# Performance work log

Measured on AMD Instinct MI355X. Metric: run time of the kernel, lower is better.

Reference implementation:

```python
import jax, jax.numpy as jnp
import numpy as np

DEPTH = 6

def sparsemax(z):
    # sparsemax over last axis (Martins & Astudillo 2016)
    z_sorted = -jnp.sort(-z, axis=-1)
    z_cum = jnp.cumsum(z_sorted, axis=-1)
    k = jnp.arange(1, z.shape[-1] + 1, dtype=z.dtype)
    support = k * z_sorted > z_cum - 1.0
    k_sup = jnp.sum(support, axis=-1, keepdims=True).astype(jnp.int32)
    tau_sum = jnp.take_along_axis(z_cum, k_sup - 1, axis=-1)
    tau = (tau_sum - 1.0) / k_sup.astype(z.dtype)
    return jnp.maximum(z - tau, 0.0)

def sparsemoid(x):
    return jnp.clip(0.5 * x + 0.5, 0.0, 1.0)

def make_bin_codes(depth):
    indices = jnp.arange(2 ** depth)
    offsets = 2 ** jnp.arange(depth)
    bin_codes = ((indices[None, :] // offsets[:, None]) % 2).astype(jnp.float32)
    return jnp.stack([bin_codes, 1.0 - bin_codes], axis=-1)  # [depth, 2^depth, 2]

def odste_forward(x, fsl, esl, thr, lt, resp, codes):
    # x: [B,J,D]; fsl: [n,t,J]; esl: [n,t,J,D]; thr/lt: [n,t]; resp: [n,c,D,2^t]
    fs = sparsemax(fsl)                               # [n,t,J]
    es = sparsemax(esl)                               # [n,t,J,D]
    sel = jnp.einsum('bjd,ntj->bntd', x, fs)          # feature selection
    sel = sel * jnp.sum(es, axis=2)[None]             # einsum 'bntd,ntjd->bntd'
    tl = (sel - thr[None, :, :, None]) * jnp.exp(-lt)[None, :, :, None]
    tl = jnp.stack([-tl, tl], axis=-1)                # [b,n,t,d,2]
    bins = sparsemoid(tl)
    bm = jnp.einsum('bntds,tcs->bntdc', bins, codes)  # [b,n,t,d,c]
    rw = jnp.prod(bm, axis=2)                         # [b,n,d,c]
    return jnp.einsum('bnds,ncds->bnd', rw, resp)     # [b,n,d]


def setup_inputs() -> dict:
    key = jax.random.key(0)
    B, D, n, t, c_tree = 64, 32, 128, DEPTH, 1
    Js = [64, 192, 320]
    ks = jax.random.split(key, 1 + 5 * len(Js))
    inp = {'x': jax.random.normal(ks[0], (B, Js[0], D), dtype=jnp.float32)}
    for i, J in enumerate(Js):
        k0, k1, k2, k3, k4 = ks[1 + 5 * i:6 + 5 * i]
        inp[f'fsl_{i}'] = jax.random.uniform(k0, (n, t, J), dtype=jnp.float32)
        inp[f'esl_{i}'] = jax.random.normal(k1, (n, t, J, D), dtype=jnp.float32)
        inp[f'thr_{i}'] = jax.random.normal(k2, (n, t), dtype=jnp.float32)
        inp[f'lt_{i}'] = jax.random.normal(k3, (n, t), dtype=jnp.float32)
        inp[f'resp_{i}'] = jax.random.normal(k4, (n, c_tree, D, 2 ** t), dtype=jnp.float32)
    return inp


def reference(x, fsl_0, esl_0, thr_0, lt_0, resp_0,
              fsl_1, esl_1, thr_1, lt_1, resp_1,
              fsl_2, esl_2, thr_2, lt_2, resp_2):
    codes = make_bin_codes(DEPTH)
    layers = [(fsl_0, esl_0, thr_0, lt_0, resp_0),
              (fsl_1, esl_1, thr_1, lt_1, resp_1),
              (fsl_2, esl_2, thr_2, lt_2, resp_2)]
    for fsl, esl, thr, lt, resp in layers:
        h = odste_forward(x, fsl, esl, thr, lt, resp, codes)
        x = jnp.concatenate([x, h], axis=1)
    return x
```

## Files before the change

### kernel.cpp

```cpp
#include <hip/hip_runtime.h>

#define OUT_COLS 448
#define OUT_STRIDE (OUT_COLS * 32)
#define NTREES 128
#define TDEPTH 6
#define NT (NTREES * TDEPTH)
#define DD 32
#define BB 64
#define PADW 64

template <int CTRL, int RMASK = 0xf, bool BC = true>
__device__ __forceinline__ float dppf(float v) {
    return __int_as_float(
        __builtin_amdgcn_update_dpp(0, __float_as_int(v), CTRL, RMASK, 0xf, BC));
}

__device__ __forceinline__ float wred64(float x) {
    x += dppf<0x111>(x);
    x += dppf<0x112>(x);
    x += dppf<0x114>(x);
    x += dppf<0x118>(x);
    x += __int_as_float(__builtin_amdgcn_update_dpp(0, __float_as_int(x), 0x142, 0xa, 0xf, false));
    x += __int_as_float(__builtin_amdgcn_update_dpp(0, __float_as_int(x), 0x143, 0xc, 0xf, false));
    return __int_as_float(__builtin_amdgcn_readlane(__float_as_int(x), 63));
}

template <int J>
__device__ __forceinline__ void fs_row(const float* __restrict__ zr, int lane,
                                       float2* __restrict__ fjv, int* __restrict__ fcnt_p) {
    constexpr int T = J / 64;
    float z[T];
    #pragma unroll
    for (int t = 0; t < T; ++t) z[t] = zr[t * 64 + lane];
    float sp = 0.f;
    #pragma unroll
    for (int t = 0; t < T; ++t) sp += z[t];
    float k = (float)J;
    float tau = (wred64(sp) - 1.f) / k;
    #pragma unroll 1
    for (int it = 0; it < 64; ++it) {
        float s2 = 0.f, c2 = 0.f;
        #pragma unroll
        for (int t = 0; t < T; ++t) {
            bool g = z[t] > tau;
            s2 += g ? z[t] : 0.f;
            c2 += g ? 1.f : 0.f;
        }
        float S2 = wred64(s2);
        float K2 = wred64(c2);
        if (K2 == k) break;
        k = K2;
        tau = (S2 - 1.f) / K2;
    }
    unsigned long long below = (1ull << lane) - 1ull;
    int base = 0;
    #pragma unroll
    for (int t = 0; t < T; ++t) {
        bool sup = z[t] > tau;
        unsigned long long m = __ballot(sup);
        int pos = base + __popcll(m & below);
        if (sup && pos < PADW)
            fjv[pos] = make_float2(__int_as_float((t * 64 + lane) * 128), z[t] - tau);
        base += __popcll(m);
    }
    int cnt = base < PADW ? base : PADW;
    for (int i = cnt + lane; i < PADW; i += 64)
        fjv[i] = make_float2(__int_as_float(0), 0.f);
    if (lane == 0) *fcnt_p = cnt;
}

template <int S>
__device__ __forceinline__ void bstep(float* a, int lane) {
    constexpr int half = 16 >> S;
    bool up = ((lane >> S) & 1) != 0;
    #pragma unroll
    for (int q = 0; q < half; ++q) {
        float send = up ? a[q] : a[half + q];
        float recv;
        if constexpr (S == 0)      recv = dppf<0xB1>(send);
        else if constexpr (S == 1) recv = dppf<0x4E>(send);
        else recv = __int_as_float(__builtin_amdgcn_ds_swizzle(
                        __float_as_int(send), ((1 << S) << 10) | 0x1F));
        float keep = up ? a[half + q] : a[q];
        a[q] = keep + recv;
    }
}

__global__ __launch_bounds__(256)
void prep_kernel(const float* __restrict__ x,
                 const float* __restrict__ f0, const float* __restrict__ f1,
                 const float* __restrict__ f2,
                 const float* __restrict__ e0, const float* __restrict__ e1,
                 const float* __restrict__ e2,
                 float2* __restrict__ fjv, int* __restrict__ fcnt,
                 float* __restrict__ part, float* __restrict__ out) {
    int w = blockIdx.x * 4 + (threadIdx.x >> 6);
    int lane = threadIdx.x & 63;

    if (w < 512) {
        const float4* x4 = (const float4*)x;
        float4* o4 = (float4*)out;
        int g = w * 64 + lane;
        int b = g >> 9, r = g & 511;
        o4[(size_t)b * (OUT_STRIDE / 4) + r] = x4[g];
        return;
    }
    w -= 512;
    if (w < 3 * NT) {
        if (w < NT) {
            fs_row<64>(f0 + (size_t)w * 64, lane, fjv + (size_t)w * PADW, fcnt + w);
        } else if (w < 2 * NT) {
            int r = w - NT;
            fs_row<192>(f1 + (size_t)r * 192, lane,
                        fjv + (size_t)(NT + r) * PADW, fcnt + NT + r);
        } else {
            int r = w - 2 * NT;
            fs_row<320>(f2 + (size_t)r * 320, lane,
                        fjv + (size_t)(2 * NT + r) * PADW, fcnt + 2 * NT + r);
        }
        return;
    }
    w -= 3 * NT;
    const float* esl; int row, chunk, J; size_t grow;
    if (w < NT)          { esl = e0; row = w; chunk = 0; J = 64; grow = (size_t)row; }
    else if (w < 4 * NT) { int q = w - NT; esl = e1; row = q / 3; chunk = q - row * 3; J = 192; grow = (size_t)(NT + row); }
    else                 { int q = w - 4 * NT; esl = e2; row = q / 5; chunk = q - row * 5; J = 320; grow = (size_t)(2 * NT + row); }

    const float4* zp4 = (const float4*)(esl + ((size_t)row * J + chunk * 64 + lane) * 32);
    float z[32];
    #pragma unroll
    for (int i = 0; i < 8; ++i) {
        float4 v = zp4[i];
        z[4 * i] = v.x; z[4 * i + 1] = v.y; z[4 * i + 2] = v.z; z[4 * i + 3] = v.w;
    }
    float mx = z[0];
    #pragma unroll
    for (int i = 1; i < 32; ++i) mx = fmaxf(mx, z[i]);
    float tau = mx - 1.0f;
    int kprev = -1;
    #pragma unroll 1
    for (int it = 0; it < 40; ++it) {
        float s0 = 0.f, s1 = 0.f, s2 = 0.f, s3 = 0.f;
        int k0 = 0, k1 = 0, k2 = 0, k3 = 0;
        #pragma unroll
        for (int i = 0; i < 8; ++i) {
            bool g0 = z[4 * i]     > tau; s0 += g0 ? z[4 * i]     : 0.f; k0 += g0;
            bool g1 = z[4 * i + 1] > tau; s1 += g1 ? z[4 * i + 1] : 0.f; k1 += g1;
            bool g2 = z[4 * i + 2] > tau; s2 += g2 ? z[4 * i + 2] : 0.f; k2 += g2;
            bool g3 = z[4 * i + 3] > tau; s3 += g3 ? z[4 * i + 3] : 0.f; k3 += g3;
        }
        float S = (s0 + s1) + (s2 + s3);
        int k = (k0 + k1) + (k2 + k3);
        bool chg = (k != kprev);
        kprev = k;
        tau = (S - 1.0f) / (float)k;
        if (__ballot(chg) == 0ull) break;
    }
    #pragma unroll
    for (int i = 0; i < 32; ++i) z[i] = fmaxf(z[i] - tau, 0.f);
    bstep<0>(z, lane);
    bstep<1>(z, lane);
    bstep<2>(z, lane);
    bstep<3>(z, lane);
    bstep<4>(z, lane);
    z[0] += __shfl_xor(z[0], 32, 64);
    if (lane < 32) {
        int d = ((lane & 1) << 4) | ((lane & 2) << 2) | (lane & 4)
              | ((lane & 8) >> 2) | ((lane & 16) >> 4);
        part[(grow * 5 + chunk) * 32 + d] = z[0];
    }
}

__global__ __launch_bounds__(256)
void main_kernel(const float2* __restrict__ fjvL, const int* __restrict__ fcnt,
                 const float* __restrict__ partL, int nch,
                 const float* __restrict__ thr, const float* __restrict__ lt,
                 const float* __restrict__ resp,
                 float* __restrict__ out, int colOff) {
    int n = blockIdx.x;
    int tid = threadIdx.x;
    __shared__ float4 s_jv[TDEPTH][PADW / 2];
    __shared__ float2 s_resp2[DD][33];
    __shared__ float  s_ess[TDEPTH][DD];
    __shared__ float  s_thr[TDEPTH], s_elt[TDEPTH];
    __shared__ int    s_cnt[TDEPTH];

    {
        const float4* g = (const float4*)(fjvL + (size_t)n * TDEPTH * PADW);
        if (tid < 192) ((float4*)s_jv)[tid] = g[tid];
    }
    {
        const float2* g = (const float2*)(resp + (size_t)n * (DD * 64));
        for (int i = tid; i < DD * 32; i += 256)
            s_resp2[i >> 5][i & 31] = g[i];
    }
    if (tid < TDEPTH * DD) {
        int t = tid >> 5, d = tid & 31;
        float e = 0.f;
        #pragma unroll
        for (int c = 0; c < 5; ++c)
            if (c < nch) e += partL[((size_t)(n * TDEPTH + t) * 5 + c) * 32 + d];
        s_ess[t][d] = e;
    }
    if (tid < TDEPTH) {
        int r = n * TDEPTH + tid;
        s_thr[tid] = thr[r];
        s_elt[tid] = expf(-lt[r]);
        s_cnt[tid] = fcnt[r];
    }
    __syncthreads();

    int b = blockIdx.y * 8 + (tid >> 5);
    int d = tid & 31;
    const char* xbd = (const char*)(out + (size_t)b * OUT_STRIDE + d);

    int maxc = s_cnt[0];
    #pragma unroll
    for (int t = 1; t < TDEPTH; ++t) maxc = max(maxc, s_cnt[t]);
    int rounds = (maxc + 7) >> 3;

    float acc0 = 0.f, acc1 = 0.f, acc2 = 0.f, acc3 = 0.f, acc4 = 0.f, acc5 = 0.f;
    for (int r = 0; r < rounds; ++r) {
        int p4 = r * 4;
        #pragma unroll
        for (int t = 0; t < TDEPTH; ++t) {
            float4 q0 = s_jv[t][p4 + 0];
            float4 q1 = s_jv[t][p4 + 1];
            float4 q2 = s_jv[t][p4 + 2];
            float4 q3 = s_jv[t][p4 + 3];
            float x0 = *(const float*)(xbd + __float_as_int(q0.x));
            float x1 = *(const float*)(xbd + __float_as_int(q0.z));
            float x2 = *(const float*)(xbd + __float_as_int(q1.x));
            float x3 = *(const float*)(xbd + __float_as_int(q1.z));
            float x4 = *(const float*)(xbd + __float_as_int(q2.x));
            float x5 = *(const float*)(xbd + __float_as_int(q2.z));
            float x6 = *(const float*)(xbd + __float_as_int(q3.x));
            float x7 = *(const float*)(xbd + __float_as_int(q3.z));
            float a = ((x0 * q0.y + x1 * q0.w) + (x2 * q1.y + x3 * q1.w))
                    + ((x4 * q2.y + x5 * q2.w) + (x6 * q3.y + x7 * q3.w));
            if (t == 0) acc0 += a;
            if (t == 1) acc1 += a;
            if (t == 2) acc2 += a;
            if (t == 3) acc3 += a;
            if (t == 4) acc4 += a;
            if (t == 5) acc5 += a;
        }
    }
    float sv[TDEPTH];
    {
        float accs[TDEPTH] = {acc0, acc1, acc2, acc3, acc4, acc5};
        #pragma unroll
        for (int t = 0; t < TDEPTH; ++t) {
            float sel = accs[t] * s_ess[t][d];
            float tlv = (sel - s_thr[t]) * s_elt[t];
            sv[t] = fminf(fmaxf(0.5f * tlv + 0.5f, 0.f), 1.f);
        }
    }

    float A[8], Bv[8];
    {
        float a0 = sv[0], a1 = 1.f - sv[0];
        float b0 = sv[1], b1 = 1.f - sv[1];
        float c0 = sv[2], c1 = 1.f - sv[2];
        A[0] = a0 * b0 * c0; A[1] = a1 * b0 * c0;
        A[2] = a0 * b1 * c0; A[3] = a1 * b1 * c0;
        A[4] = a0 * b0 * c1; A[5] = a1 * b0 * c1;
        A[6] = a0 * b1 * c1; A[7] = a1 * b1 * c1;
        float d0 = sv[3], d1 = 1.f - sv[3];
        float e0 = sv[4], e1 = 1.f - sv[4];
        float f0 = sv[5], f1 = 1.f - sv[5];
        Bv[0] = d0 * e0 * f0; Bv[1] = d1 * e0 * f0;
        Bv[2] = d0 * e1 * f0; Bv[3] = d1 * e1 * f0;
        Bv[4] = d0 * e0 * f1; Bv[5] = d1 * e0 * f1;
        Bv[6] = d0 * e1 * f1; Bv[7] = d1 * e1 * f1;
    }
    float o = 0.f;
    #pragma unroll
    for (int c2 = 0; c2 < 8; ++c2) {
        float2 r0 = s_resp2[d][(8 * c2) >> 1];
        float2 r1 = s_resp2[d][(8 * c2 + 2) >> 1];
        float2 r2 = s_resp2[d][(8 * c2 + 4) >> 1];
        float2 r3 = s_resp2[d][(8 * c2 + 6) >> 1];
        float inner = (A[0] * r0.x + A[1] * r0.y) + (A[2] * r1.x + A[3] * r1.y)
                    + (A[4] * r2.x + A[5] * r2.y) + (A[6] * r3.x + A[7] * r3.y);
        o += Bv[c2] * inner;
    }
    out[(size_t)b * OUT_STRIDE + (size_t)(colOff + n) * DD + d] = o;
}

extern "C" void kernel_launch(void* const* d_in, const int* in_sizes, int n_in,
                              void* d_out, int out_size, void* d_ws, size_t ws_size,
                              hipStream_t stream) {
    const float* x = (const float*)d_in[0];
    float* out = (float*)d_out;

    const size_t NPAD = (size_t)3 * NT * PADW;
    char* ws = (char*)d_ws;
    float2* fjv  = (float2*)(ws);
    int*    fcnt = (int*)(ws + NPAD * 8);
    float*  part = (float*)(ws + NPAD * 8 + 16384);

    prep_kernel<<<9728 / 4, 256, 0, stream>>>(
        x,
        (const float*)d_in[1], (const float*)d_in[6], (const float*)d_in[11],
        (const float*)d_in[2], (const float*)d_in[7], (const float*)d_in[12],
        fjv, fcnt, part, out);

    const int nchs[3] = {1, 3, 5};
    int colOff = 64;
    for (int L = 0; L < 3; ++L) {
        const float* thr  = (const float*)d_in[3 + 5 * L];
        const float* lt   = (const float*)d_in[4 + 5 * L];
        const float* resp = (const float*)d_in[5 + 5 * L];
        main_kernel<<<dim3(NTREES, 8), 256, 0, stream>>>(
            fjv + (size_t)L * NT * PADW, fcnt + L * NT,
            part + (size_t)L * NT * 5 * 32, nchs[L],
            thr, lt, resp, out, colOff);
        colOff += NTREES;
    }
}
```

Before: 56.92 us.

## Defer later-layer esl sparsemax tasks into the preceding main-kernel launches

```diff
diff --git a/kernel.cpp b/kernel.cpp
--- a/kernel.cpp
+++ b/kernel.cpp
@@ -86,6 +86,61 @@
     }
 }
 
+__device__ __forceinline__ void es_task(int w, int lane,
+                                        const float* __restrict__ e0,
+                                        const float* __restrict__ e1,
+                                        const float* __restrict__ e2,
+                                        float* __restrict__ part) {
+    const float* esl; int row, chunk, J; size_t grow;
+    if (w < NT)          { esl = e0; row = w; chunk = 0; J = 64; grow = (size_t)row; }
+    else if (w < 4 * NT) { int q = w - NT; esl = e1; row = q / 3; chunk = q - row * 3; J = 192; grow = (size_t)(NT + row); }
+    else                 { int q = w - 4 * NT; esl = e2; row = q / 5; chunk = q - row * 5; J = 320; grow = (size_t)(2 * NT + row); }
+
+    const float4* zp4 = (const float4*)(esl + ((size_t)row * J + chunk * 64 + lane) * 32);
+    float z[32];
+    #pragma unroll
+    for (int i = 0; i < 8; ++i) {
+        float4 v = zp4[i];
+        z[4 * i] = v.x; z[4 * i + 1] = v.y; z[4 * i + 2] = v.z; z[4 * i + 3] = v.w;
+    }
+    float mx = z[0];
+    #pragma unroll
+    for (int i = 1; i < 32; ++i) mx = fmaxf(mx, z[i]);
+    float tau = mx - 1.0f;
+    int kprev = -1;
+    #pragma unroll 1
+    for (int it = 0; it < 40; ++it) {
+        float s0 = 0.f, s1 = 0.f, s2 = 0.f, s3 = 0.f;
+        int k0 = 0, k1 = 0, k2 = 0, k3 = 0;
+        #pragma unroll
+        for (int i = 0; i < 8; ++i) {
+            bool g0 = z[4 * i]     > tau; s0 += g0 ? z[4 * i]     : 0.f; k0 += g0;
+            bool g1 = z[4 * i + 1] > tau; s1 += g1 ? z[4 * i + 1] : 0.f; k1 += g1;
+            bool g2 = z[4 * i + 2] > tau; s2 += g2 ? z[4 * i + 2] : 0.f; k2 += g2;
+            bool g3 = z[4 * i + 3] > tau; s3 += g3 ? z[4 * i + 3] : 0.f; k3 += g3;
+        }
+        float S = (s0 + s1) + (s2 + s3);
+        int k = (k0 + k1) + (k2 + k3);
+        bool chg = (k != kprev);
+        kprev = k;
+        tau = (S - 1.0f) / (float)k;
+        if (__ballot(chg) == 0ull) break;
+    }
+    #pragma unroll
+    for (int i = 0; i < 32; ++i) z[i] = fmaxf(z[i] - tau, 0.f);
+    bstep<0>(z, lane);
+    bstep<1>(z, lane);
+    bstep<2>(z, lane);
+    bstep<3>(z, lane);
+    bstep<4>(z, lane);
+    z[0] += __shfl_xor(z[0], 32, 64);
+    if (lane < 32) {
+        int d = ((lane & 1) << 4) | ((lane & 2) << 2) | (lane & 4)
+              | ((lane & 8) >> 2) | ((lane & 16) >> 4);
+        part[(grow * 5 + chunk) * 32 + d] = z[0];
+    }
+}
+
 __global__ __launch_bounds__(256)
 void prep_kernel(const float* __restrict__ x,
                  const float* __restrict__ f0, const float* __restrict__ f1,
@@ -93,7 +148,7 @@
                  const float* __restrict__ e0, const float* __restrict__ e1,
                  const float* __restrict__ e2,
                  float2* __restrict__ fjv, int* __restrict__ fcnt,
-                 float* __restrict__ part, float* __restrict__ out) {
+                 float* __restrict__ part, float* __restrict__ out, int esEnd) {
     int w = blockIdx.x * 4 + (threadIdx.x >> 6);
     int lane = threadIdx.x & 63;
 
@@ -121,64 +176,26 @@
         return;
     }
     w -= 3 * NT;
-    const float* esl; int row, chunk, J; size_t grow;
-    if (w < NT)          { esl = e0; row = w; chunk = 0; J = 64; grow = (size_t)row; }
-    else if (w < 4 * NT) { int q = w - NT; esl = e1; row = q / 3; chunk = q - row * 3; J = 192; grow = (size_t)(NT + row); }
-    else                 { int q = w - 4 * NT; esl = e2; row = q / 5; chunk = q - row * 5; J = 320; grow = (size_t)(2 * NT + row); }
-
-    const float4* zp4 = (const float4*)(esl + ((size_t)row * J + chunk * 64 + lane) * 32);
-    float z[32];
-    #pragma unroll
-    for (int i = 0; i < 8; ++i) {
-        float4 v = zp4[i];
-        z[4 * i] = v.x; z[4 * i + 1] = v.y; z[4 * i + 2] = v.z; z[4 * i + 3] = v.w;
-    }
-    float mx = z[0];
-    #pragma unroll
-    for (int i = 1; i < 32; ++i) mx = fmaxf(mx, z[i]);
-    float tau = mx - 1.0f;
-    int kprev = -1;
-    #pragma unroll 1
-    for (int it = 0; it < 40; ++it) {
-        float s0 = 0.f, s1 = 0.f, s2 = 0.f, s3 = 0.f;
-        int k0 = 0, k1 = 0, k2 = 0, k3 = 0;
-        #pragma unroll
-        for (int i = 0; i < 8; ++i) {
-            bool g0 = z[4 * i]     > tau; s0 += g0 ? z[4 * i]     : 0.f; k0 += g0;
-            bool g1 = z[4 * i + 1] > tau; s1 += g1 ? z[4 * i + 1] : 0.f; k1 += g1;
-            bool g2 = z[4 * i + 2] > tau; s2 += g2 ? z[4 * i + 2] : 0.f; k2 += g2;
-            bool g3 = z[4 * i + 3] > tau; s3 += g3 ? z[4 * i + 3] : 0.f; k3 += g3;
-        }
-        float S = (s0 + s1) + (s2 + s3);
-        int k = (k0 + k1) + (k2 + k3);
-        bool chg = (k != kprev);
-        kprev = k;
-        tau = (S - 1.0f) / (float)k;
-        if (__ballot(chg) == 0ull) break;
-    }
-    #pragma unroll
-    for (int i = 0; i < 32; ++i) z[i] = fmaxf(z[i] - tau, 0.f);
-    bstep<0>(z, lane);
-    bstep<1>(z, lane);
-    bstep<2>(z, lane);
-    bstep<3>(z, lane);
-    bstep<4>(z, lane);
-    z[0] += __shfl_xor(z[0], 32, 64);
-    if (lane < 32) {
-        int d = ((lane & 1) << 4) | ((lane & 2) << 2) | (lane & 4)
-              | ((lane & 8) >> 2) | ((lane & 16) >> 4);
-        part[(grow * 5 + chunk) * 32 + d] = z[0];
-    }
+    if (w < esEnd) es_task(w, lane, e0, e1, e2, part);
 }
 
 __global__ __launch_bounds__(256)
-void main_kernel(const float2* __restrict__ fjvL, const int* __restrict__ fcnt,
-                 const float* __restrict__ partL, int nch,
-                 const float* __restrict__ thr, const float* __restrict__ lt,
-                 const float* __restrict__ resp,
-                 float* __restrict__ out, int colOff) {
-    int n = blockIdx.x;
+void mainplus_kernel(const float2* __restrict__ fjvL, const int* __restrict__ fcnt,
+                     const float* __restrict__ partL, int nch,
+                     const float* __restrict__ thr, const float* __restrict__ lt,
+                     const float* __restrict__ resp,
+                     float* __restrict__ out, int colOff,
+                     const float* __restrict__ e0, const float* __restrict__ e1,
+                     const float* __restrict__ e2, float* __restrict__ partAll,
+                     int nMain, int esBeg, int esEnd) {
     int tid = threadIdx.x;
+    if ((int)blockIdx.x >= nMain) {
+        int w = esBeg + (blockIdx.x - nMain) * 4 + (tid >> 6);
+        if (w < esEnd) es_task(w, tid & 63, e0, e1, e2, partAll);
+        return;
+    }
+    int n = blockIdx.x & (NTREES - 1);
+    int by = blockIdx.x >> 7;
     __shared__ float4 s_jv[TDEPTH][PADW / 2];
     __shared__ float2 s_resp2[DD][33];
     __shared__ float  s_ess[TDEPTH][DD];
@@ -210,7 +227,7 @@
     }
     __syncthreads();
 
-    int b = blockIdx.y * 8 + (tid >> 5);
+    int b = by * 8 + (tid >> 5);
     int d = tid & 31;
     const char* xbd = (const char*)(out + (size_t)b * OUT_STRIDE + d);
 
@@ -300,11 +317,17 @@
     int*    fcnt = (int*)(ws + NPAD * 8);
     float*  part = (float*)(ws + NPAD * 8 + 16384);
 
-    prep_kernel<<<9728 / 4, 256, 0, stream>>>(
+    const float* e0 = (const float*)d_in[2];
+    const float* e1 = (const float*)d_in[7];
+    const float* e2 = (const float*)d_in[12];
+
+    const int ES_A = 2304;
+    const int ES_B = 4608;
+
+    prep_kernel<<<5120 / 4, 256, 0, stream>>>(
         x,
         (const float*)d_in[1], (const float*)d_in[6], (const float*)d_in[11],
-        (const float*)d_in[2], (const float*)d_in[7], (const float*)d_in[12],
-        fjv, fcnt, part, out);
+        e0, e1, e2, fjv, fcnt, part, out, ES_A);
 
     const int nchs[3] = {1, 3, 5};
     int colOff = 64;
@@ -312,10 +335,14 @@
         const float* thr  = (const float*)d_in[3 + 5 * L];
         const float* lt   = (const float*)d_in[4 + 5 * L];
         const float* resp = (const float*)d_in[5 + 5 * L];
-        main_kernel<<<dim3(NTREES, 8), 256, 0, stream>>>(
+        int esBeg = (L == 0) ? ES_A : (L == 1) ? ES_B : 0;
+        int esEnd = (L == 0) ? ES_B : (L == 1) ? 6912 : 0;
+        int nEsBlocks = (esEnd - esBeg + 3) / 4;
+        mainplus_kernel<<<1024 + nEsBlocks, 256, 0, stream>>>(
             fjv + (size_t)L * NT * PADW, fcnt + L * NT,
             part + (size_t)L * NT * 5 * 32, nchs[L],
-            thr, lt, resp, out, colOff);
+            thr, lt, resp, out, colOff,
+            e0, e1, e2, part, 1024, esBeg, esEnd);
         colOff += NTREES;
     }
 }
```

New measurement: 59.22 us. 4.0% more time.

## Split esl sparsemax rows across 8-lane groups with coalesced float4 loads

Applied to the files above, without the earlier changes.

```diff
diff --git a/kernel.cpp b/kernel.cpp
--- a/kernel.cpp
+++ b/kernel.cpp
@@ -14,6 +14,12 @@
     return __int_as_float(
         __builtin_amdgcn_update_dpp(0, __float_as_int(v), CTRL, RMASK, 0xf, BC));
 }
+
+__device__ __forceinline__ float swx1(float v)  { return dppf<0xB1>(v); }
+__device__ __forceinline__ float swx2(float v)  { return dppf<0x4E>(v); }
+__device__ __forceinline__ float swx4(float v)  { return __int_as_float(__builtin_amdgcn_ds_swizzle(__float_as_int(v), 0x101F)); }
+__device__ __forceinline__ float swx8(float v)  { return __int_as_float(__builtin_amdgcn_ds_swizzle(__float_as_int(v), 0x201F)); }
+__device__ __forceinline__ float swx16(float v) { return __int_as_float(__builtin_amdgcn_ds_swizzle(__float_as_int(v), 0x401F)); }
 
 __device__ __forceinline__ float wred64(float x) {
     x += dppf<0x111>(x);
@@ -69,20 +75,55 @@
     if (lane == 0) *fcnt_p = cnt;
 }
 
-template <int S>
-__device__ __forceinline__ void bstep(float* a, int lane) {
-    constexpr int half = 16 >> S;
-    bool up = ((lane >> S) & 1) != 0;
-    #pragma unroll
-    for (int q = 0; q < half; ++q) {
-        float send = up ? a[q] : a[half + q];
-        float recv;
-        if constexpr (S == 0)      recv = dppf<0xB1>(send);
-        else if constexpr (S == 1) recv = dppf<0x4E>(send);
-        else recv = __int_as_float(__builtin_amdgcn_ds_swizzle(
-                        __float_as_int(send), ((1 << S) << 10) | 0x1F));
-        float keep = up ? a[half + q] : a[q];
-        a[q] = keep + recv;
+__device__ __forceinline__ void es_task(int w, int lane,
+                                        const float* __restrict__ e0,
+                                        const float* __restrict__ e1,
+                                        const float* __restrict__ e2,
+                                        float* __restrict__ part) {
+    const float* esl; int row, chunk, J; size_t grow;
+    if (w < NT)          { esl = e0; row = w; chunk = 0; J = 64; grow = (size_t)row; }
+    else if (w < 4 * NT) { int q = w - NT; esl = e1; row = q / 3; chunk = q - row * 3; J = 192; grow = (size_t)(NT + row); }
+    else                 { int q = w - 4 * NT; esl = e2; row = q / 5; chunk = q - row * 5; J = 320; grow = (size_t)(2 * NT + row); }
+
+    const float4* zp4 = (const float4*)(esl + ((size_t)row * J + chunk * 64) * 32);
+    float4 acc = make_float4(0.f, 0.f, 0.f, 0.f);
+    #pragma unroll
+    for (int p = 0; p < 8; ++p) {
+        float4 v = zp4[p * 64 + lane];
+        float mx = fmaxf(fmaxf(v.x, v.y), fmaxf(v.z, v.w));
+        mx = fmaxf(mx, swx1(mx));
+        mx = fmaxf(mx, swx2(mx));
+        mx = fmaxf(mx, swx4(mx));
+        float tau = mx - 1.0f;
+        float kprev = -1.0f;
+        #pragma unroll 1
+        for (int it = 0; it < 40; ++it) {
+            float s  = (v.x > tau ? v.x : 0.f) + (v.y > tau ? v.y : 0.f)
+                     + (v.z > tau ? v.z : 0.f) + (v.w > tau ? v.w : 0.f);
+            float kc = (v.x > tau ? 1.f : 0.f) + (v.y > tau ? 1.f : 0.f)
+                     + (v.z > tau ? 1.f : 0.f) + (v.w > tau ? 1.f : 0.f);
+            s += swx1(s);   kc += swx1(kc);
+            s += swx2(s);   kc += swx2(kc);
+            s += swx4(s);   kc += swx4(kc);
+            bool chg = (kc != kprev);
+            kprev = kc;
+            tau = (s - 1.0f) / kc;
+            if (__ballot(chg) == 0ull) break;
+        }
+        acc.x += fmaxf(v.x - tau, 0.f);
+        acc.y += fmaxf(v.y - tau, 0.f);
+        acc.z += fmaxf(v.z - tau, 0.f);
+        acc.w += fmaxf(v.w - tau, 0.f);
+    }
+    acc.x += swx8(acc.x);  acc.y += swx8(acc.y);  acc.z += swx8(acc.z);  acc.w += swx8(acc.w);
+    acc.x += swx16(acc.x); acc.y += swx16(acc.y); acc.z += swx16(acc.z); acc.w += swx16(acc.w);
+    acc.x += __shfl_xor(acc.x, 32, 64);
+    acc.y += __shfl_xor(acc.y, 32, 64);
+    acc.z += __shfl_xor(acc.z, 32, 64);
+    acc.w += __shfl_xor(acc.w, 32, 64);
+    if (lane < 8) {
+        float4* p4 = (float4*)(part + (grow * 5 + chunk) * 32);
+        p4[lane] = acc;
     }
 }
 
@@ -121,54 +162,7 @@
         return;
     }
     w -= 3 * NT;
-    const float* esl; int row, chunk, J; size_t grow;
-    if (w < NT)          { esl = e0; row = w; chunk = 0; J = 64; grow = (size_t)row; }
-    else if (w < 4 * NT) { int q = w - NT; esl = e1; row = q / 3; chunk = q - row * 3; J = 192; grow = (size_t)(NT + row); }
-    else                 { int q = w - 4 * NT; esl = e2; row = q / 5; chunk = q - row * 5; J = 320; grow = (size_t)(2 * NT + row); }
-
-    const float4* zp4 = (const float4*)(esl + ((size_t)row * J + chunk * 64 + lane) * 32);
-    float z[32];
-    #pragma unroll
-    for (int i = 0; i < 8; ++i) {
-        float4 v = zp4[i];
-        z[4 * i] = v.x; z[4 * i + 1] = v.y; z[4 * i + 2] = v.z; z[4 * i + 3] = v.w;
-    }
-    float mx = z[0];
-    #pragma unroll
-    for (int i = 1; i < 32; ++i) mx = fmaxf(mx, z[i]);
-    float tau = mx - 1.0f;
-    int kprev = -1;
-    #pragma unroll 1
-    for (int it = 0; it < 40; ++it) {
-        float s0 = 0.f, s1 = 0.f, s2 = 0.f, s3 = 0.f;
-        int k0 = 0, k1 = 0, k2 = 0, k3 = 0;
-        #pragma unroll
-        for (int i = 0; i < 8; ++i) {
-            bool g0 = z[4 * i]     > tau; s0 += g0 ? z[4 * i]     : 0.f; k0 += g0;
-            bool g1 = z[4 * i + 1] > tau; s1 += g1 ? z[4 * i + 1] : 0.f; k1 += g1;
-            bool g2 = z[4 * i + 2] > tau; s2 += g2 ? z[4 * i + 2] : 0.f; k2 += g2;
-            bool g3 = z[4 * i + 3] > tau; s3 += g3 ? z[4 * i + 3] : 0.f; k3 += g3;
-        }
-        float S = (s0 + s1) + (s2 + s3);
-        int k = (k0 + k1) + (k2 + k3);
-        bool chg = (k != kprev);
-        kprev = k;
-        tau = (S - 1.0f) / (float)k;
-        if (__ballot(chg) == 0ull) break;
-    }
-    #pragma unroll
-    for (int i = 0; i < 32; ++i) z[i] = fmaxf(z[i] - tau, 0.f);
-    bstep<0>(z, lane);
-    bstep<1>(z, lane);
-    bstep<2>(z, lane);
-    bstep<3>(z, lane);
-    bstep<4>(z, lane);
-    z[0] += __shfl_xor(z[0], 32, 64);
-    if (lane < 32) {
-        int d = ((lane & 1) << 4) | ((lane & 2) << 2) | (lane & 4)
-              | ((lane & 8) >> 2) | ((lane & 16) >> 4);
-        part[(grow * 5 + chunk) * 32 + d] = z[0];
-    }
+    es_task(w, lane, e0, e1, e2, part);
 }
 
 __global__ __launch_bounds__(256)
```

Result: slower. 62.85 us (+10.4%).
